# Kernel tuning notes

Hardware: AMD Instinct MI355X
Metric: run time of the kernel (lower is better)

## Reference

```python
import math
import jax, jax.numpy as jnp
import numpy as np

NHID = 1024
HEADS = 16
SEQ = 1024
BATCH = 8


def setup_inputs() -> dict:
    key = jax.random.key(0)
    ks = jax.random.split(key, 12)
    s = 0.02
    inp = {
        "query": jax.random.normal(ks[0], (SEQ, BATCH, NHID), jnp.float32),
        "key": jax.random.normal(ks[1], (SEQ, BATCH, NHID), jnp.float32),
        "value": jax.random.normal(ks[2], (SEQ, BATCH, NHID), jnp.float32),
        "qs_p": jax.random.normal(ks[3], (1, 1, NHID), jnp.float32) * s,
        "ks_p": jax.random.normal(ks[4], (1, 1, NHID), jnp.float32) * s,
        "vs_p": jax.random.normal(ks[5], (1, 1, NHID), jnp.float32) * s,
        "Wq": jax.random.normal(ks[6], (NHID, NHID), jnp.float32) * s,
        "bq": jax.random.normal(ks[7], (NHID,), jnp.float32) * s,
        "Wzf": jax.random.normal(ks[8], (2 * NHID, NHID), jnp.float32) * s,
        "bzf": jax.random.normal(ks[9], (2 * NHID,), jnp.float32) * s,
    }
    # additive causal mask, viewed as (1,1,S,S) and added to scores
    causal = jnp.triu(jnp.ones((SEQ, SEQ), jnp.float32), k=1) * (-1e9)
    inp["attn_mask"] = causal
    return inp


def reference(query, key, value, qs_p, ks_p, vs_p, Wq, bq, Wzf, bzf, attn_mask):
    nhid = NHID
    heads = HEADS
    dim = nhid // heads

    # sigmoid gates on Q/K/V scales
    qs = jax.nn.sigmoid(qs_p)              # (1,1,nhid)
    ks_g = jax.nn.sigmoid(ks_p)
    vs_in = jax.nn.sigmoid(vs_p)

    # QRNNLayer(window=1, output_gate=False) on single-step vs:
    # z = tanh(Wz vs + bz), f = sigmoid(Wf vs + bf), h = f * z (h0 = 0)
    zf = jnp.einsum('abn,mn->abm', vs_in, Wzf) + bzf   # (1,1,2*nhid)
    z = jnp.tanh(zf[..., :nhid])
    f = jax.nn.sigmoid(zf[..., nhid:])
    vs = f * z                                          # (1,1,nhid)

    # q projection (k,v have no Linear with defaults)
    q_lin = jnp.einsum('sbn,mn->sbm', query, Wq) + bq

    q = qs * q_lin       # (S,B,nhid)
    k = ks_g * key
    v = vs * value

    # seq-first -> batch-first, split heads
    def split_heads(t):
        t = t.transpose(1, 0, 2)                         # (B,S,nhid)
        B, S, _ = t.shape
        return t.reshape(B, S, heads, dim).transpose(0, 2, 1, 3)  # (B,H,S,d)

    qh, kh, vh = split_heads(q), split_heads(k), split_heads(v)

    scores = jnp.einsum('bhqd,bhkd->bhqk', qh, kh) / math.sqrt(dim)
    scores = scores + attn_mask[None, None]              # (B,H,S,S)
    weights = jax.nn.softmax(scores, axis=-1)
    mix = jnp.einsum('bhqk,bhkd->bhqd', weights, vh)     # (B,H,S,d)

    B = mix.shape[0]
    mix = mix.transpose(0, 2, 1, 3).reshape(B, -1, nhid)  # (B,S,nhid)
    mix = mix.transpose(1, 0, 2)                          # (S,B,nhid) seq-first
    return mix, weights
```

## Files before the change

### kernel.cpp

```cpp
#include <hip/hip_runtime.h>

typedef unsigned short u16;
typedef unsigned int   u32;
typedef float  f32x4  __attribute__((ext_vector_type(4)));
typedef short  bf16x8 __attribute__((ext_vector_type(8)));
typedef unsigned short u16x8 __attribute__((ext_vector_type(8)));
typedef unsigned short u16x4 __attribute__((ext_vector_type(4)));
typedef unsigned int   u32x2 __attribute__((ext_vector_type(2)));

#define DEV __device__ __forceinline__

constexpr int S  = 1024;
constexpr int BB = 8;
constexpr int NH = 1024;
constexpr int H  = 16;

DEV u16 f2bf(float f) {
  union { float f; unsigned u; } v{f};
  unsigned r = v.u + 0x7FFFu + ((v.u >> 16) & 1u);
  return (u16)(r >> 16);
}
DEV float sigm(float x) { return 1.0f / (1.0f + __expf(-x)); }
DEV float exp2a(float x) { float r; asm("v_exp_f32 %0, %1" : "=v"(r) : "v"(x)); return r; }

DEV void gload_lds16(const void* g, void* l) {
  __builtin_amdgcn_global_load_lds(
      (const __attribute__((address_space(1))) unsigned int*)g,
      (__attribute__((address_space(3))) unsigned int*)l, 16, 0, 0);
}

DEV f32x4 ntload4(const float* p) {
  return __builtin_nontemporal_load((const f32x4*)p);
}
DEV void ntstore4(f32x4 v, float* p) {
  __builtin_nontemporal_store(v, (f32x4*)p);
}

__global__ __launch_bounds__(256) void k_gates(
    const float* __restrict__ qs_p, const float* __restrict__ ks_p,
    const float* __restrict__ vs_p, const float* __restrict__ Wq,
    const float* __restrict__ bq,  const float* __restrict__ Wzf,
    const float* __restrict__ bzf,
    float* __restrict__ ksg, float* __restrict__ vsg,
    float* __restrict__ bq2, u16* __restrict__ wq_bf)
{
  int m = blockIdx.x * 4 + (threadIdx.x >> 6);
  int l = threadIdx.x & 63;
  const float* wz = Wzf + (size_t)m * NH;
  const float* wf = Wzf + (size_t)(m + NH) * NH;
  int base = l * 16;
  float za = 0.f, fa = 0.f;
#pragma unroll
  for (int i = 0; i < 16; i += 4) {
    f32x4 vp  = *(const f32x4*)(vs_p + base + i);
    f32x4 wzv = *(const f32x4*)(wz + base + i);
    f32x4 wfv = *(const f32x4*)(wf + base + i);
    float v0 = sigm(vp.x), v1 = sigm(vp.y), v2 = sigm(vp.z), v3 = sigm(vp.w);
    za += v0 * wzv.x + v1 * wzv.y + v2 * wzv.z + v3 * wzv.w;
    fa += v0 * wfv.x + v1 * wfv.y + v2 * wfv.z + v3 * wfv.w;
  }
#pragma unroll
  for (int off = 1; off < 64; off <<= 1) {
    za += __shfl_xor(za, off);
    fa += __shfl_xor(fa, off);
  }
  float z   = tanhf(za + bzf[m]);
  float f   = sigm(fa + bzf[m + NH]);
  float qsm = sigm(qs_p[m]);
  if (l == 0) {
    ksg[m] = sigm(ks_p[m]);
    vsg[m] = f * z;
    bq2[m] = qsm * bq[m];
  }
  const float* wqr = Wq + (size_t)m * NH;
  u16* dst = wq_bf + (size_t)m * NH + base;
#pragma unroll
  for (int i = 0; i < 16; i += 4) {
    f32x4 wv = *(const f32x4*)(wqr + base + i);
    u16x4 o;
    o[0] = f2bf(qsm * wv.x); o[1] = f2bf(qsm * wv.y);
    o[2] = f2bf(qsm * wv.z); o[3] = f2bf(qsm * wv.w);
    *(u16x4*)(dst + i) = o;
  }
}

__global__ __launch_bounds__(256) void k_prep(
    const float* __restrict__ query, const float* __restrict__ key,
    const float* __restrict__ value, const float* __restrict__ ksg,
    const float* __restrict__ vsg,
    u16* __restrict__ qx, u16* __restrict__ kout, u16* __restrict__ vout)
{
  __shared__ float tile[64][65];
  size_t idx = ((size_t)blockIdx.x * 256 + threadIdx.x) * 8;
  {
    f32x4 a = ntload4(query + idx);
    f32x4 b = ntload4(query + idx + 4);
    u16x8 o;
    o[0] = f2bf(a.x); o[1] = f2bf(a.y); o[2] = f2bf(a.z); o[3] = f2bf(a.w);
    o[4] = f2bf(b.x); o[5] = f2bf(b.y); o[6] = f2bf(b.z); o[7] = f2bf(b.w);
    *(u16x8*)(qx + idx) = o;
  }
  {
    int n0 = (int)(idx & 1023);
    int b  = (int)((idx >> 10) & 7);
    int s  = (int)(idx >> 13);
    f32x4 a  = ntload4(key + idx);
    f32x4 c  = ntload4(key + idx + 4);
    f32x4 g0 = *(const f32x4*)(ksg + n0);
    f32x4 g1 = *(const f32x4*)(ksg + n0 + 4);
    int h = n0 >> 6, d0 = n0 & 63;
    u16* dst = kout + (((size_t)(b * H + h) * S + s) * 64 + d0);
    u16x8 o;
    o[0] = f2bf(a.x * g0.x); o[1] = f2bf(a.y * g0.y);
    o[2] = f2bf(a.z * g0.z); o[3] = f2bf(a.w * g0.w);
    o[4] = f2bf(c.x * g1.x); o[5] = f2bf(c.y * g1.y);
    o[6] = f2bf(c.z * g1.z); o[7] = f2bf(c.w * g1.w);
    *(u16x8*)dst = o;
  }
  if (blockIdx.x < 2048) {
    int bh = blockIdx.x >> 4, kt = blockIdx.x & 15;
    int b = bh >> 4, h = bh & 15;
    int t = threadIdx.x;
    int sp = t >> 2, c0 = (t & 3) * 16;
    const float* src = value + ((size_t)(kt * 64 + sp) * (BB * NH) + b * NH + h * 64 + c0);
#pragma unroll
    for (int i = 0; i < 16; i += 4) {
      f32x4 v = ntload4(src + i);
      f32x4 g = *(const f32x4*)(vsg + h * 64 + c0 + i);
      tile[sp][c0 + i + 0] = v.x * g.x;
      tile[sp][c0 + i + 1] = v.y * g.y;
      tile[sp][c0 + i + 2] = v.z * g.z;
      tile[sp][c0 + i + 3] = v.w * g.w;
    }
    __syncthreads();
    int d = t >> 2, s0 = (t & 3) * 16;
    u16* dst = vout + (((size_t)bh * 16 + kt) * 64 + d) * 64 + s0;
    u16x8 o0, o1;
#pragma unroll
    for (int i = 0; i < 8; ++i) o0[i] = f2bf(tile[s0 + i][d]);
#pragma unroll
    for (int i = 0; i < 8; ++i) o1[i] = f2bf(tile[s0 + 8 + i][d]);
    *(u16x8*)dst       = o0;
    *(u16x8*)(dst + 8) = o1;
  }
}

__global__ __launch_bounds__(256) void k_gemm_q(
    const u16* __restrict__ qx, const u16* __restrict__ wq,
    const float* __restrict__ bq2, u16* __restrict__ qws,
    float* __restrict__ wout)
{
  __shared__ __align__(16) u16 As[128 * 64];
  __shared__ __align__(16) u16 Bs[128 * 64];
  int bid = blockIdx.x;
  int swz = (bid & 7) * 64 + (bid >> 3);
  int bx = swz & 7, by = swz >> 3;
  int tid = threadIdx.x, w = tid >> 6, l = tid & 63;
  int wr = w >> 1, wc = w & 1;
  f32x4 zero4 = {0.f, 0.f, 0.f, 0.f};
  f32x4 acc[4][4];
#pragma unroll
  for (int fi = 0; fi < 4; ++fi)
#pragma unroll
    for (int fj = 0; fj < 4; ++fj) acc[fi][fj] = zero4;

  for (int kt = 0; kt < 16; ++kt) {
    __syncthreads();
#pragma unroll
    for (int ii = 0; ii < 4; ++ii) {
      int i = w * 4 + ii;
      int row = i * 8 + (l >> 3);
      int blk = (l & 7) ^ (row & 7);
      gload_lds16(qx + ((size_t)(by * 128 + row) * 1024 + kt * 64 + blk * 8), &As[i * 512]);
      gload_lds16(wq + ((size_t)(bx * 128 + row) * 1024 + kt * 64 + blk * 8), &Bs[i * 512]);
    }
#pragma unroll
    for (int c2 = 0; c2 < 4; ++c2) {
      int c = kt * 4 + c2;
      if (c < 56) {
        int ti = c >> 3;
        int tile_id = bid * 7 + ti;
        if (tile_id < 3328) {
          int fbh = tile_id / 26;
          int r = tile_id - fbh * 26;
          int t2 = (r < 14) ? 0 : 1;
          int j = t2 ? (r - 10) : (r + 2);
          int q = ((c & 7) << 8) + tid;
          float* dst = wout + (size_t)fbh * S * S + (size_t)(t2 * 128 + (q >> 4)) * S
                       + j * 64 + (q & 15) * 4;
          ntstore4(zero4, dst);
        }
      }
    }
    __syncthreads();
#pragma unroll
    for (int kk = 0; kk < 2; ++kk) {
      bf16x8 av[4], bv[4];
#pragma unroll
      for (int f = 0; f < 4; ++f) {
        int ar = wr * 64 + f * 16 + (l & 15);
        av[f] = *(const bf16x8*)&As[ar * 64 + ((((kk << 2) + (l >> 4)) ^ (ar & 7)) << 3)];
        int br = wc * 64 + f * 16 + (l & 15);
        bv[f] = *(const bf16x8*)&Bs[br * 64 + ((((kk << 2) + (l >> 4)) ^ (br & 7)) << 3)];
      }
#pragma unroll
      for (int fi = 0; fi < 4; ++fi)
#pragma unroll
        for (int fj = 0; fj < 4; ++fj)
          acc[fi][fj] = __builtin_amdgcn_mfma_f32_16x16x32_bf16(av[fi], bv[fj], acc[fi][fj], 0, 0, 0);
    }
  }
  const float SC = 0.18033688f;
#pragma unroll
  for (int fi = 0; fi < 4; ++fi) {
    int grb = by * 128 + wr * 64 + fi * 16 + ((l >> 4) << 2);
#pragma unroll
    for (int fj = 0; fj < 4; ++fj) {
      int mcol = bx * 128 + wc * 64 + fj * 16 + (l & 15);
      float badd = bq2[mcol];
      int h = mcol >> 6, d = mcol & 63;
#pragma unroll
      for (int r = 0; r < 4; ++r) {
        int gr = grb + r;
        int srow = gr >> 3, bb = gr & 7;
        qws[((size_t)(bb * H + h) * S + srow) * 64 + d] = f2bf((acc[fi][fj][r] + badd) * SC);
      }
    }
  }
}

__global__ __launch_bounds__(512, 4) void k_attn(
    const u16* __restrict__ qws, const u16* __restrict__ kws,
    const u16* __restrict__ vtw, float* __restrict__ mix,
    float* __restrict__ wout)
{
  __shared__ __align__(16) u16 KV[4][64 * 64];
  __shared__ __align__(16) u16 Ps[8][16 * 64];
  int bid = blockIdx.x;
  int swz = (bid & 7) * 128 + (bid >> 3);
  int t = swz & 7, bh = swz >> 3;
  int tid = threadIdx.x, w = tid >> 6, l = tid & 63;
  int g = l >> 4, lq = l & 15;
  int q0 = t * 128;
  int myq = q0 + 16 * w + lq;
  int jmax = 2 * t + 1;
  int jd = 2 * t + (w >> 2);
  float* wbase = wout + (size_t)bh * S * S;
  u16* KVf = &KV[0][0];
  int srow = l >> 3, sblk = l & 7;

  auto stageK = [&](int j, int buf) {
    int row = w * 8 + srow;
    int blk = sblk ^ (row & 7);
    gload_lds16(kws + ((size_t)bh * S + j * 64 + row) * 64 + blk * 8,
                &KVf[buf * 4096 + w * 512]);
  };
  auto stageV = [&](int j, int buf) {
    int row = w * 8 + srow;
    int blk = sblk ^ (row & 7);
    gload_lds16(vtw + (((size_t)bh * 16 + j) * 64 + row) * 64 + blk * 8,
                &KVf[buf * 4096 + w * 512]);
  };

#pragma unroll
  for (int ii = 0; ii < 2; ++ii) {
    int i = w * 2 + ii;
    int row = i * 8 + srow;
    int blk = sblk ^ (row & 7);
    gload_lds16(qws + ((size_t)bh * S + q0 + row) * 64 + blk * 8, &KVf[i * 512]);
  }
  asm volatile("s_waitcnt vmcnt(0)" ::: "memory");
  __builtin_amdgcn_sched_barrier(0);
  bf16x8 qa[2];
#pragma unroll
  for (int kk = 0; kk < 2; ++kk) {
    int qr = 16 * w + lq;
    qa[kk] = *(const bf16x8*)&KVf[qr * 64 + ((((kk << 2) + g) ^ (qr & 7)) << 3)];
  }
  asm volatile("s_waitcnt lgkmcnt(0)" ::: "memory");
  __builtin_amdgcn_sched_barrier(0);
  __builtin_amdgcn_s_barrier();

  stageK(0, 0);
  if (jmax >= 1) stageK(1, 1);
  if (jmax >= 2) stageK(2, 2);
  float lsum = 0.f;
  for (int j = 0; j <= jmax; ++j) {
    if (j + 2 <= jmax)      asm volatile("s_waitcnt vmcnt(2)" ::: "memory");
    else if (j + 1 <= jmax) asm volatile("s_waitcnt vmcnt(1)" ::: "memory");
    else                    asm volatile("s_waitcnt vmcnt(0)" ::: "memory");
    __builtin_amdgcn_sched_barrier(0);
    __builtin_amdgcn_s_barrier();
    __builtin_amdgcn_sched_barrier(0);
    if (j + 3 <= jmax) stageK(j + 3, (j + 3) & 3);
    __builtin_amdgcn_sched_barrier(0);
    if (j <= jd) {
      int jb = (j & 3) * 4096;
      f32x4 sacc[4];
      f32x4 zero4 = {0.f, 0.f, 0.f, 0.f};
#pragma unroll
      for (int fj = 0; fj < 4; ++fj) sacc[fj] = zero4;
      __builtin_amdgcn_s_setprio(1);
#pragma unroll
      for (int kk = 0; kk < 2; ++kk)
#pragma unroll
        for (int fj = 0; fj < 4; ++fj) {
          int kr = fj * 16 + lq;
          bf16x8 kb = *(const bf16x8*)&KVf[jb + kr * 64 + ((((kk << 2) + g) ^ (kr & 7)) << 3)];
          sacc[fj] = __builtin_amdgcn_mfma_f32_16x16x32_bf16(kb, qa[kk], sacc[fj], 0, 0, 0);
        }
      __builtin_amdgcn_s_setprio(0);
      if (j < jd) {
#pragma unroll
        for (int fj = 0; fj < 4; ++fj)
#pragma unroll
          for (int r = 0; r < 4; ++r) lsum += exp2a(sacc[fj][r]);
      } else {
#pragma unroll
        for (int fj = 0; fj < 4; ++fj)
#pragma unroll
          for (int r = 0; r < 4; ++r) {
            int ki = j * 64 + fj * 16 + 4 * g + r;
            if (ki <= myq) lsum += exp2a(sacc[fj][r]);
          }
      }
    }
  }
  lsum += __shfl_xor(lsum, 16);
  lsum += __shfl_xor(lsum, 32);
  float invl = 1.0f / lsum;

  __builtin_amdgcn_s_barrier();

  stageK(0, 0);
  stageV(0, 2);
  int cur = 0;
  f32x4 oacc[4];
  {
    f32x4 zero4 = {0.f, 0.f, 0.f, 0.f};
#pragma unroll
    for (int db = 0; db < 4; ++db) oacc[db] = zero4;
  }
  char* pb = (char*)&Ps[w][0];
  int pswz = (lq & 7) * 16;
  for (int j = 0; j <= jmax; ++j) {
    if (j == 0) asm volatile("s_waitcnt vmcnt(0)" ::: "memory");
    else        asm volatile("s_waitcnt vmcnt(4)" ::: "memory");
    __builtin_amdgcn_sched_barrier(0);
    __builtin_amdgcn_s_barrier();
    __builtin_amdgcn_sched_barrier(0);
    if (j < jmax) { stageK(j + 1, cur ^ 1); stageV(j + 1, 2 + (cur ^ 1)); }
    __builtin_amdgcn_sched_barrier(0);
    if (j > jd) {
      f32x4 z4 = {0.f, 0.f, 0.f, 0.f};
#pragma unroll
      for (int fj = 0; fj < 4; ++fj)
        ntstore4(z4, wbase + (size_t)myq * S + j * 64 + fj * 16 + g * 4);
    } else {
      int kbase = cur * 4096;
      f32x4 sacc[4];
      f32x4 zero4 = {0.f, 0.f, 0.f, 0.f};
#pragma unroll
      for (int fj = 0; fj < 4; ++fj) sacc[fj] = zero4;
      __builtin_amdgcn_s_setprio(1);
#pragma unroll
      for (int kk = 0; kk < 2; ++kk)
#pragma unroll
        for (int fj = 0; fj < 4; ++fj) {
          int kr = fj * 16 + lq;
          bf16x8 kb = *(const bf16x8*)&KVf[kbase + kr * 64 + ((((kk << 2) + g) ^ (kr & 7)) << 3)];
          sacc[fj] = __builtin_amdgcn_mfma_f32_16x16x32_bf16(kb, qa[kk], sacc[fj], 0, 0, 0);
        }
      __builtin_amdgcn_s_setprio(0);
      bool diag = (j == jd);
      float p0[4], p1[4], p2[4], p3[4];
#pragma unroll
      for (int fj = 0; fj < 4; ++fj) {
        float* pp = fj == 0 ? p0 : fj == 1 ? p1 : fj == 2 ? p2 : p3;
#pragma unroll
        for (int r = 0; r < 4; ++r) {
          float e = exp2a(sacc[fj][r]) * invl;
          if (diag) {
            int ki = j * 64 + fj * 16 + 4 * g + r;
            if (ki > myq) e = 0.f;
          }
          pp[r] = e;
        }
      }
#pragma unroll
      for (int fj = 0; fj < 4; ++fj) {
        float* pp = fj == 0 ? p0 : fj == 1 ? p1 : fj == 2 ? p2 : p3;
        u32 w0, w1;
        asm("v_cvt_pk_bf16_f32 %0, %1, %2" : "=v"(w0) : "v"(pp[0]), "v"(pp[1]));
        asm("v_cvt_pk_bf16_f32 %0, %1, %2" : "=v"(w1) : "v"(pp[2]), "v"(pp[3]));
        u32x2 wv = {w0, w1};
        *(u32x2*)(pb + lq * 128 + ((fj * 32 + g * 8) ^ pswz)) = wv;
      }
#pragma unroll
      for (int fj = 0; fj < 4; ++fj) {
        float* pp = fj == 0 ? p0 : fj == 1 ? p1 : fj == 2 ? p2 : p3;
        f32x4 f4 = {pp[0], pp[1], pp[2], pp[3]};
        ntstore4(f4, wbase + (size_t)myq * S + j * 64 + fj * 16 + g * 4);
      }
      asm volatile("s_waitcnt lgkmcnt(0)" ::: "memory");
      __builtin_amdgcn_sched_barrier(0);
      __builtin_amdgcn_s_setprio(1);
#pragma unroll
      for (int kk = 0; kk < 2; ++kk) {
        bf16x8 pa = *(const bf16x8*)(pb + lq * 128 + ((kk * 64 + g * 16) ^ pswz));
#pragma unroll
        for (int db = 0; db < 4; ++db) {
          int d = db * 16 + lq;
          bf16x8 vb = *(const bf16x8*)&KVf[(2 + cur) * 4096 + d * 64 + ((((kk << 2) + g) ^ (d & 7)) << 3)];
          oacc[db] = __builtin_amdgcn_mfma_f32_16x16x32_bf16(pa, vb, oacc[db], 0, 0, 0);
        }
      }
      __builtin_amdgcn_s_setprio(0);
    }
    cur ^= 1;
  }

  int b = bh >> 4, h = bh & 15;
#pragma unroll
  for (int db = 0; db < 4; ++db) {
#pragma unroll
    for (int r = 0; r < 4; ++r) {
      int qi = q0 + 16 * w + 4 * g + r;
      __builtin_nontemporal_store(oacc[db][r],
          mix + (size_t)(qi * BB + b) * NH + h * 64 + db * 16 + lq);
    }
  }

  if (t >= 2) {
    f32x4 z4 = {0.f, 0.f, 0.f, 0.f};
    int cstart = (jmax + 1) * 64;
    for (int lr = 0; lr < 16; ++lr) {
      float* rowp = wbase + (size_t)(q0 + 16 * w + lr) * S;
      for (int c = cstart + l * 4; c < S; c += 256)
        ntstore4(z4, rowp + c);
    }
  }
}

extern "C" void kernel_launch(void* const* d_in, const int* in_sizes, int n_in,
                              void* d_out, int out_size, void* d_ws, size_t ws_size,
                              hipStream_t stream) {
  (void)in_sizes; (void)n_in; (void)out_size; (void)ws_size;
  const float* query = (const float*)d_in[0];
  const float* key   = (const float*)d_in[1];
  const float* value = (const float*)d_in[2];
  const float* qs_p  = (const float*)d_in[3];
  const float* ks_p  = (const float*)d_in[4];
  const float* vs_p  = (const float*)d_in[5];
  const float* Wq    = (const float*)d_in[6];
  const float* bq    = (const float*)d_in[7];
  const float* Wzf   = (const float*)d_in[8];
  const float* bzf   = (const float*)d_in[9];

  char* ws = (char*)d_ws;
  float* ksg  = (float*)(ws + 0x1000);
  float* vsg  = (float*)(ws + 0x2000);
  float* bq2  = (float*)(ws + 0x3000);
  u16* wq_bf  = (u16*)(ws + 0x4000);
  u16* qx_bf  = (u16*)(ws + 0x204000);
  u16* q_ws   = (u16*)(ws + 0x1204000);
  u16* k_ws   = (u16*)(ws + 0x2204000);
  u16* vt_ws  = (u16*)(ws + 0x3204000);

  float* mix  = (float*)d_out;
  float* wout = mix + (size_t)S * BB * NH;

  k_gates<<<256, 256, 0, stream>>>(qs_p, ks_p, vs_p, Wq, bq, Wzf, bzf,
                                   ksg, vsg, bq2, wq_bf);
  k_prep<<<4096, 256, 0, stream>>>(query, key, value, ksg, vsg,
                                   qx_bf, k_ws, vt_ws);
  k_gemm_q<<<512, 256, 0, stream>>>(qx_bf, wq_bf, bq2, q_ws, wout);
  k_attn<<<1024, 512, 0, stream>>>(q_ws, k_ws, vt_ws, mix, wout);
}
```

Before: 227.3 us.

## Fuse Q projection GEMM into attention kernel and gates into prep

Merges the gate computation into the prep kernel as extra blocks, applying the K sigmoid gate inline and deferring the V scale to the attention output. The separate Q projection GEMM is removed: each attention block now computes its own 128x64 Q tile from bf16 query and the head's weight slice, double-buffered in LDS, before the flash loop. This cuts two launches and the Q workspace round trip. In exchange the zero-fill of the upper weights region moves entirely into the attention tail. There is also a dependency hazard: the prep kernel writes vsg, bq2 and wq_bf from the same launch that other blocks run in, although attn only reads them after prep finishes, so ordering is fine.

```diff
diff --git a/kernel.cpp b/kernel.cpp
--- a/kernel.cpp
+++ b/kernel.cpp
@@ -36,61 +36,59 @@
   __builtin_nontemporal_store(v, (f32x4*)p);
 }
 
-__global__ __launch_bounds__(256) void k_gates(
-    const float* __restrict__ qs_p, const float* __restrict__ ks_p,
-    const float* __restrict__ vs_p, const float* __restrict__ Wq,
-    const float* __restrict__ bq,  const float* __restrict__ Wzf,
-    const float* __restrict__ bzf,
-    float* __restrict__ ksg, float* __restrict__ vsg,
-    float* __restrict__ bq2, u16* __restrict__ wq_bf)
-{
-  int m = blockIdx.x * 4 + (threadIdx.x >> 6);
-  int l = threadIdx.x & 63;
-  const float* wz = Wzf + (size_t)m * NH;
-  const float* wf = Wzf + (size_t)(m + NH) * NH;
-  int base = l * 16;
-  float za = 0.f, fa = 0.f;
-#pragma unroll
-  for (int i = 0; i < 16; i += 4) {
-    f32x4 vp  = *(const f32x4*)(vs_p + base + i);
-    f32x4 wzv = *(const f32x4*)(wz + base + i);
-    f32x4 wfv = *(const f32x4*)(wf + base + i);
-    float v0 = sigm(vp.x), v1 = sigm(vp.y), v2 = sigm(vp.z), v3 = sigm(vp.w);
-    za += v0 * wzv.x + v1 * wzv.y + v2 * wzv.z + v3 * wzv.w;
-    fa += v0 * wfv.x + v1 * wfv.y + v2 * wfv.z + v3 * wfv.w;
-  }
-#pragma unroll
-  for (int off = 1; off < 64; off <<= 1) {
-    za += __shfl_xor(za, off);
-    fa += __shfl_xor(fa, off);
-  }
-  float z   = tanhf(za + bzf[m]);
-  float f   = sigm(fa + bzf[m + NH]);
-  float qsm = sigm(qs_p[m]);
-  if (l == 0) {
-    ksg[m] = sigm(ks_p[m]);
-    vsg[m] = f * z;
-    bq2[m] = qsm * bq[m];
-  }
-  const float* wqr = Wq + (size_t)m * NH;
-  u16* dst = wq_bf + (size_t)m * NH + base;
-#pragma unroll
-  for (int i = 0; i < 16; i += 4) {
-    f32x4 wv = *(const f32x4*)(wqr + base + i);
-    u16x4 o;
-    o[0] = f2bf(qsm * wv.x); o[1] = f2bf(qsm * wv.y);
-    o[2] = f2bf(qsm * wv.z); o[3] = f2bf(qsm * wv.w);
-    *(u16x4*)(dst + i) = o;
-  }
-}
+constexpr float SC = 0.18033688f;
 
 __global__ __launch_bounds__(256) void k_prep(
     const float* __restrict__ query, const float* __restrict__ key,
-    const float* __restrict__ value, const float* __restrict__ ksg,
-    const float* __restrict__ vsg,
-    u16* __restrict__ qx, u16* __restrict__ kout, u16* __restrict__ vout)
+    const float* __restrict__ value, const float* __restrict__ qs_p,
+    const float* __restrict__ ks_p,  const float* __restrict__ vs_p,
+    const float* __restrict__ Wq,   const float* __restrict__ bq,
+    const float* __restrict__ Wzf,  const float* __restrict__ bzf,
+    u16* __restrict__ qx, u16* __restrict__ kout, u16* __restrict__ vout,
+    float* __restrict__ vsg, float* __restrict__ bq2, u16* __restrict__ wq_bf)
 {
   __shared__ float tile[64][65];
+  if (blockIdx.x >= 4096) {
+    int m = (blockIdx.x - 4096) * 4 + (threadIdx.x >> 6);
+    int l = threadIdx.x & 63;
+    const float* wz = Wzf + (size_t)m * NH;
+    const float* wf = Wzf + (size_t)(m + NH) * NH;
+    int base = l * 16;
+    float za = 0.f, fa = 0.f;
+#pragma unroll
+    for (int i = 0; i < 16; i += 4) {
+      f32x4 vp  = *(const f32x4*)(vs_p + base + i);
+      f32x4 wzv = *(const f32x4*)(wz + base + i);
+      f32x4 wfv = *(const f32x4*)(wf + base + i);
+      float v0 = sigm(vp.x), v1 = sigm(vp.y), v2 = sigm(vp.z), v3 = sigm(vp.w);
+      za += v0 * wzv.x + v1 * wzv.y + v2 * wzv.z + v3 * wzv.w;
+      fa += v0 * wfv.x + v1 * wfv.y + v2 * wfv.z + v3 * wfv.w;
+    }
+#pragma unroll
+    for (int off = 1; off < 64; off <<= 1) {
+      za += __shfl_xor(za, off);
+      fa += __shfl_xor(fa, off);
+    }
+    float z   = tanhf(za + bzf[m]);
+    float f   = sigm(fa + bzf[m + NH]);
+    float qsm = sigm(qs_p[m]);
+    if (l == 0) {
+      vsg[m] = f * z;
+      bq2[m] = qsm * bq[m] * SC;
+    }
+    float qss = qsm * SC;
+    const float* wqr = Wq + (size_t)m * NH;
+    u16* dst = wq_bf + (size_t)m * NH + base;
+#pragma unroll
+    for (int i = 0; i < 16; i += 4) {
+      f32x4 wv = *(const f32x4*)(wqr + base + i);
+      u16x4 o;
+      o[0] = f2bf(qss * wv.x); o[1] = f2bf(qss * wv.y);
+      o[2] = f2bf(qss * wv.z); o[3] = f2bf(qss * wv.w);
+      *(u16x4*)(dst + i) = o;
+    }
+    return;
+  }
   size_t idx = ((size_t)blockIdx.x * 256 + threadIdx.x) * 8;
   {
     f32x4 a = ntload4(query + idx);
@@ -106,15 +104,15 @@
     int s  = (int)(idx >> 13);
     f32x4 a  = ntload4(key + idx);
     f32x4 c  = ntload4(key + idx + 4);
-    f32x4 g0 = *(const f32x4*)(ksg + n0);
-    f32x4 g1 = *(const f32x4*)(ksg + n0 + 4);
+    f32x4 k0 = *(const f32x4*)(ks_p + n0);
+    f32x4 k1 = *(const f32x4*)(ks_p + n0 + 4);
     int h = n0 >> 6, d0 = n0 & 63;
     u16* dst = kout + (((size_t)(b * H + h) * S + s) * 64 + d0);
     u16x8 o;
-    o[0] = f2bf(a.x * g0.x); o[1] = f2bf(a.y * g0.y);
-    o[2] = f2bf(a.z * g0.z); o[3] = f2bf(a.w * g0.w);
-    o[4] = f2bf(c.x * g1.x); o[5] = f2bf(c.y * g1.y);
-    o[6] = f2bf(c.z * g1.z); o[7] = f2bf(c.w * g1.w);
+    o[0] = f2bf(a.x * sigm(k0.x)); o[1] = f2bf(a.y * sigm(k0.y));
+    o[2] = f2bf(a.z * sigm(k0.z)); o[3] = f2bf(a.w * sigm(k0.w));
+    o[4] = f2bf(c.x * sigm(k1.x)); o[5] = f2bf(c.y * sigm(k1.y));
+    o[6] = f2bf(c.z * sigm(k1.z)); o[7] = f2bf(c.w * sigm(k1.w));
     *(u16x8*)dst = o;
   }
   if (blockIdx.x < 2048) {
@@ -126,11 +124,10 @@
 #pragma unroll
     for (int i = 0; i < 16; i += 4) {
       f32x4 v = ntload4(src + i);
-      f32x4 g = *(const f32x4*)(vsg + h * 64 + c0 + i);
-      tile[sp][c0 + i + 0] = v.x * g.x;
-      tile[sp][c0 + i + 1] = v.y * g.y;
-      tile[sp][c0 + i + 2] = v.z * g.z;
-      tile[sp][c0 + i + 3] = v.w * g.w;
+      tile[sp][c0 + i + 0] = v.x;
+      tile[sp][c0 + i + 1] = v.y;
+      tile[sp][c0 + i + 2] = v.z;
+      tile[sp][c0 + i + 3] = v.w;
     }
     __syncthreads();
     int d = t >> 2, s0 = (t & 3) * 16;
@@ -145,100 +142,18 @@
   }
 }
 
-__global__ __launch_bounds__(256) void k_gemm_q(
-    const u16* __restrict__ qx, const u16* __restrict__ wq,
-    const float* __restrict__ bq2, u16* __restrict__ qws,
-    float* __restrict__ wout)
+__global__ __launch_bounds__(512, 4) void k_attn(
+    const u16* __restrict__ qx, const u16* __restrict__ wqb,
+    const float* __restrict__ bq2, const u16* __restrict__ kws,
+    const u16* __restrict__ vtw, const float* __restrict__ vsg,
+    float* __restrict__ mix, float* __restrict__ wout)
 {
-  __shared__ __align__(16) u16 As[128 * 64];
-  __shared__ __align__(16) u16 Bs[128 * 64];
+  __shared__ __align__(16) char smem[65536];
   int bid = blockIdx.x;
-  int swz = (bid & 7) * 64 + (bid >> 3);
-  int bx = swz & 7, by = swz >> 3;
-  int tid = threadIdx.x, w = tid >> 6, l = tid & 63;
-  int wr = w >> 1, wc = w & 1;
-  f32x4 zero4 = {0.f, 0.f, 0.f, 0.f};
-  f32x4 acc[4][4];
-#pragma unroll
-  for (int fi = 0; fi < 4; ++fi)
-#pragma unroll
-    for (int fj = 0; fj < 4; ++fj) acc[fi][fj] = zero4;
-
-  for (int kt = 0; kt < 16; ++kt) {
-    __syncthreads();
-#pragma unroll
-    for (int ii = 0; ii < 4; ++ii) {
-      int i = w * 4 + ii;
-      int row = i * 8 + (l >> 3);
-      int blk = (l & 7) ^ (row & 7);
-      gload_lds16(qx + ((size_t)(by * 128 + row) * 1024 + kt * 64 + blk * 8), &As[i * 512]);
-      gload_lds16(wq + ((size_t)(bx * 128 + row) * 1024 + kt * 64 + blk * 8), &Bs[i * 512]);
-    }
-#pragma unroll
-    for (int c2 = 0; c2 < 4; ++c2) {
-      int c = kt * 4 + c2;
-      if (c < 56) {
-        int ti = c >> 3;
-        int tile_id = bid * 7 + ti;
-        if (tile_id < 3328) {
-          int fbh = tile_id / 26;
-          int r = tile_id - fbh * 26;
-          int t2 = (r < 14) ? 0 : 1;
-          int j = t2 ? (r - 10) : (r + 2);
-          int q = ((c & 7) << 8) + tid;
-          float* dst = wout + (size_t)fbh * S * S + (size_t)(t2 * 128 + (q >> 4)) * S
-                       + j * 64 + (q & 15) * 4;
-          ntstore4(zero4, dst);
-        }
-      }
-    }
-    __syncthreads();
-#pragma unroll
-    for (int kk = 0; kk < 2; ++kk) {
-      bf16x8 av[4], bv[4];
-#pragma unroll
-      for (int f = 0; f < 4; ++f) {
-        int ar = wr * 64 + f * 16 + (l & 15);
-        av[f] = *(const bf16x8*)&As[ar * 64 + ((((kk << 2) + (l >> 4)) ^ (ar & 7)) << 3)];
-        int br = wc * 64 + f * 16 + (l & 15);
-        bv[f] = *(const bf16x8*)&Bs[br * 64 + ((((kk << 2) + (l >> 4)) ^ (br & 7)) << 3)];
-      }
-#pragma unroll
-      for (int fi = 0; fi < 4; ++fi)
-#pragma unroll
-        for (int fj = 0; fj < 4; ++fj)
-          acc[fi][fj] = __builtin_amdgcn_mfma_f32_16x16x32_bf16(av[fi], bv[fj], acc[fi][fj], 0, 0, 0);
-    }
-  }
-  const float SC = 0.18033688f;
-#pragma unroll
-  for (int fi = 0; fi < 4; ++fi) {
-    int grb = by * 128 + wr * 64 + fi * 16 + ((l >> 4) << 2);
-#pragma unroll
-    for (int fj = 0; fj < 4; ++fj) {
-      int mcol = bx * 128 + wc * 64 + fj * 16 + (l & 15);
-      float badd = bq2[mcol];
-      int h = mcol >> 6, d = mcol & 63;
-#pragma unroll
-      for (int r = 0; r < 4; ++r) {
-        int gr = grb + r;
-        int srow = gr >> 3, bb = gr & 7;
-        qws[((size_t)(bb * H + h) * S + srow) * 64 + d] = f2bf((acc[fi][fj][r] + badd) * SC);
-      }
-    }
-  }
-}
-
-__global__ __launch_bounds__(512, 4) void k_attn(
-    const u16* __restrict__ qws, const u16* __restrict__ kws,
-    const u16* __restrict__ vtw, float* __restrict__ mix,
-    float* __restrict__ wout)
-{
-  __shared__ __align__(16) u16 KV[4][64 * 64];
-  __shared__ __align__(16) u16 Ps[8][16 * 64];
-  int bid = blockIdx.x;
-  int swz = (bid & 7) * 128 + (bid >> 3);
-  int t = swz & 7, bh = swz >> 3;
+  int b = bid & 7;
+  int idx = bid >> 3;
+  int h = idx & 15, t = idx >> 4;
+  int bh = b * 16 + h;
   int tid = threadIdx.x, w = tid >> 6, l = tid & 63;
   int g = l >> 4, lq = l & 15;
   int q0 = t * 128;
@@ -246,8 +161,79 @@
   int jmax = 2 * t + 1;
   int jd = 2 * t + (w >> 2);
   float* wbase = wout + (size_t)bh * S * S;
-  u16* KVf = &KV[0][0];
   int srow = l >> 3, sblk = l & 7;
+
+  u16* As = (u16*)smem;
+  u16* Bs = (u16*)(smem + 32768);
+  u16* Qs = (u16*)smem;
+  u16* KVf = (u16*)(smem + 16384);
+
+  {
+    size_t qrowbase = (size_t)(q0 * 8 + b) * 1024;
+    auto stageA = [&](int kt, int buf) {
+#pragma unroll
+      for (int ii = 0; ii < 2; ++ii) {
+        int i = w * 2 + ii;
+        int row = i * 8 + srow;
+        int blk = sblk ^ (row & 7);
+        gload_lds16(qx + qrowbase + (size_t)row * 8192 + kt * 64 + blk * 8,
+                    &As[buf * 8192 + i * 512]);
+      }
+    };
+    auto stageB = [&](int kt, int buf) {
+      int row = w * 8 + srow;
+      int blk = sblk ^ (row & 7);
+      gload_lds16(wqb + (size_t)(h * 64 + row) * 1024 + kt * 64 + blk * 8,
+                  &Bs[buf * 4096 + w * 512]);
+    };
+    f32x4 acc[4];
+    f32x4 zero4 = {0.f, 0.f, 0.f, 0.f};
+#pragma unroll
+    for (int fj = 0; fj < 4; ++fj) acc[fj] = zero4;
+    stageA(0, 0); stageB(0, 0);
+    for (int kt = 0; kt < 16; ++kt) {
+      asm volatile("s_waitcnt vmcnt(0)" ::: "memory");
+      __builtin_amdgcn_sched_barrier(0);
+      __builtin_amdgcn_s_barrier();
+      __builtin_amdgcn_sched_barrier(0);
+      if (kt < 15) { stageA(kt + 1, (kt + 1) & 1); stageB(kt + 1, (kt + 1) & 1); }
+      __builtin_amdgcn_sched_barrier(0);
+      int ab = (kt & 1) * 8192, bb = (kt & 1) * 4096;
+      __builtin_amdgcn_s_setprio(1);
+#pragma unroll
+      for (int kk = 0; kk < 2; ++kk) {
+        int ar = 16 * w + lq;
+        bf16x8 av = *(const bf16x8*)&As[ab + ar * 64 + ((((kk << 2) + g) ^ (ar & 7)) << 3)];
+#pragma unroll
+        for (int fj = 0; fj < 4; ++fj) {
+          int br = fj * 16 + lq;
+          bf16x8 bv = *(const bf16x8*)&Bs[bb + br * 64 + ((((kk << 2) + g) ^ (br & 7)) << 3)];
+          acc[fj] = __builtin_amdgcn_mfma_f32_16x16x32_bf16(av, bv, acc[fj], 0, 0, 0);
+        }
+      }
+      __builtin_amdgcn_s_setprio(0);
+    }
+    float bq4[4];
+#pragma unroll
+    for (int fj = 0; fj < 4; ++fj) bq4[fj] = bq2[h * 64 + fj * 16 + lq];
+#pragma unroll
+    for (int fj = 0; fj < 4; ++fj) {
+      int d = fj * 16 + lq;
+#pragma unroll
+      for (int r = 0; r < 4; ++r) {
+        int qrow = 16 * w + (g << 2) + r;
+        Qs[qrow * 64 + (((fj * 2 + (d >> 3 & 1)) ^ (qrow & 7)) << 3) + (d & 7)] =
+            f2bf(acc[fj][r] + bq4[fj]);
+      }
+    }
+    __syncthreads();
+  }
+  bf16x8 qa[2];
+#pragma unroll
+  for (int kk = 0; kk < 2; ++kk) {
+    int qr = 16 * w + lq;
+    qa[kk] = *(const bf16x8*)&Qs[qr * 64 + ((((kk << 2) + g) ^ (qr & 7)) << 3)];
+  }
 
   auto stageK = [&](int j, int buf) {
     int row = w * 8 + srow;
@@ -262,25 +248,6 @@
                 &KVf[buf * 4096 + w * 512]);
   };
 
-#pragma unroll
-  for (int ii = 0; ii < 2; ++ii) {
-    int i = w * 2 + ii;
-    int row = i * 8 + srow;
-    int blk = sblk ^ (row & 7);
-    gload_lds16(qws + ((size_t)bh * S + q0 + row) * 64 + blk * 8, &KVf[i * 512]);
-  }
-  asm volatile("s_waitcnt vmcnt(0)" ::: "memory");
-  __builtin_amdgcn_sched_barrier(0);
-  bf16x8 qa[2];
-#pragma unroll
-  for (int kk = 0; kk < 2; ++kk) {
-    int qr = 16 * w + lq;
-    qa[kk] = *(const bf16x8*)&KVf[qr * 64 + ((((kk << 2) + g) ^ (qr & 7)) << 3)];
-  }
-  asm volatile("s_waitcnt lgkmcnt(0)" ::: "memory");
-  __builtin_amdgcn_sched_barrier(0);
-  __builtin_amdgcn_s_barrier();
-
   stageK(0, 0);
   if (jmax >= 1) stageK(1, 1);
   if (jmax >= 2) stageK(2, 2);
@@ -341,7 +308,7 @@
 #pragma unroll
     for (int db = 0; db < 4; ++db) oacc[db] = zero4;
   }
-  char* pb = (char*)&Ps[w][0];
+  char* pb = smem + 49152 + w * 2048;
   int pswz = (lq & 7) * 16;
   for (int j = 0; j <= jmax; ++j) {
     if (j == 0) asm volatile("s_waitcnt vmcnt(0)" ::: "memory");
@@ -420,18 +387,20 @@
     cur ^= 1;
   }
 
-  int b = bh >> 4, h = bh & 15;
+  float vs4[4];
+#pragma unroll
+  for (int db = 0; db < 4; ++db) vs4[db] = vsg[h * 64 + db * 16 + lq];
 #pragma unroll
   for (int db = 0; db < 4; ++db) {
 #pragma unroll
     for (int r = 0; r < 4; ++r) {
       int qi = q0 + 16 * w + 4 * g + r;
-      __builtin_nontemporal_store(oacc[db][r],
+      __builtin_nontemporal_store(oacc[db][r] * vs4[db],
           mix + (size_t)(qi * BB + b) * NH + h * 64 + db * 16 + lq);
     }
   }
 
-  if (t >= 2) {
+  {
     f32x4 z4 = {0.f, 0.f, 0.f, 0.f};
     int cstart = (jmax + 1) * 64;
     for (int lr = 0; lr < 16; ++lr) {
@@ -458,22 +427,19 @@
   const float* bzf   = (const float*)d_in[9];
 
   char* ws = (char*)d_ws;
-  float* ksg  = (float*)(ws + 0x1000);
-  float* vsg  = (float*)(ws + 0x2000);
-  float* bq2  = (float*)(ws + 0x3000);
+  float* vsg  = (float*)(ws + 0x1000);
+  float* bq2  = (float*)(ws + 0x2000);
   u16* wq_bf  = (u16*)(ws + 0x4000);
   u16* qx_bf  = (u16*)(ws + 0x204000);
-  u16* q_ws   = (u16*)(ws + 0x1204000);
-  u16* k_ws   = (u16*)(ws + 0x2204000);
-  u16* vt_ws  = (u16*)(ws + 0x3204000);
+  u16* k_ws   = (u16*)(ws + 0x1204000);
+  u16* vt_ws  = (u16*)(ws + 0x2204000);
 
   float* mix  = (float*)d_out;
   float* wout = mix + (size_t)S * BB * NH;
 
-  k_gates<<<256, 256, 0, stream>>>(qs_p, ks_p, vs_p, Wq, bq, Wzf, bzf,
-                                   ksg, vsg, bq2, wq_bf);
-  k_prep<<<4096, 256, 0, stream>>>(query, key, value, ksg, vsg,
-                                   qx_bf, k_ws, vt_ws);
-  k_gemm_q<<<512, 256, 0, stream>>>(qx_bf, wq_bf, bq2, q_ws, wout);
-  k_attn<<<1024, 512, 0, stream>>>(q_ws, k_ws, vt_ws, mix, wout);
-}
+  k_prep<<<4352, 256, 0, stream>>>(query, key, value, qs_p, ks_p, vs_p,
+                                   Wq, bq, Wzf, bzf,
+                                   qx_bf, k_ws, vt_ws, vsg, bq2, wq_bf);
+  k_attn<<<1024, 512, 0, stream>>>(qx_bf, wq_bf, bq2, k_ws, vt_ws, vsg,
+                                   mix, wout);
+}
```

New measurement: 217.7 us. 4.3% less time.
